# Kernel tuning notes

Measured on AMD Instinct MI355X. Metric: run time of the kernel, lower is better.

Reference implementation:

```python
import jax, jax.numpy as jnp
import numpy as np

GRID_SIZE = 4
SPLINE_ORDER = 3
EDGE_DIM = 384


def make_grid():
    # efficient-KAN default grid_range [-1, 1]
    h = 2.0 / GRID_SIZE
    return (jnp.arange(-SPLINE_ORDER, GRID_SIZE + SPLINE_ORDER + 1, dtype=jnp.float32) * h - 1.0)


def b_splines(x, grid, k):
    # x: (N, d); grid: (G+2k+1,) shared across features -> (N, d, G+k)
    xe = x[..., None]
    bases = ((xe >= grid[:-1]) & (xe < grid[1:])).astype(x.dtype)
    for j in range(1, k + 1):
        bases = ((xe - grid[: -(j + 1)]) / (grid[j:-1] - grid[: -(j + 1)]) * bases[..., :-1]
                 + (grid[j + 1:] - xe) / (grid[j + 1:] - grid[1:-j]) * bases[..., 1:])
    return bases


def kan_linear(x, base_W, spline_W, grid):
    # efficient-KAN KANLinear: silu base path + spline path
    base = jax.nn.silu(x) @ base_W.T
    B = b_splines(x, grid, SPLINE_ORDER)          # (N, in, G+k)
    spline = jnp.einsum('nic,oic->no', B, spline_W)
    return base + spline


def gckan_layer(x, edge_index, edge_attr, p, grid):
    ea = edge_attr @ p['edge_W'].T + p['edge_b']          # (E, out)
    xt = x @ p['node_W'].T + p['node_b']                  # (N, out)
    row, col = edge_index[0], edge_index[1]
    msg = ea * xt[row]                                    # gather + multiply
    agg = jnp.zeros_like(xt).at[col].add(msg)             # scatter-add
    return kan_linear(agg, p['base_W'], p['spline_W'], grid)


def _layer_params(key, in_feat, out_feat):
    k1, k2, k3, k4 = jax.random.split(key, 4)
    coef = GRID_SIZE + SPLINE_ORDER
    return {
        'node_W': jax.random.normal(k1, (out_feat, in_feat), jnp.float32) / np.sqrt(in_feat),
        'node_b': jnp.zeros((out_feat,), jnp.float32),
        'edge_W': jax.random.normal(k2, (out_feat, EDGE_DIM), jnp.float32) / np.sqrt(EDGE_DIM),
        'edge_b': jnp.zeros((out_feat,), jnp.float32),
        'base_W': jax.random.normal(k3, (out_feat, out_feat), jnp.float32) / np.sqrt(out_feat),
        'spline_W': jax.random.normal(k4, (out_feat, out_feat, coef), jnp.float32) * (0.1 / np.sqrt(out_feat)),
    }


def setup_inputs() -> dict:
    N, E, F, H, C = 50000, 500000, 256, 256, 32
    key = jax.random.key(0)
    ks = jax.random.split(key, 6)
    inp = {
        'x': jax.random.normal(ks[0], (N, F), jnp.float32),
        'edge_index': jax.random.randint(ks[1], (2, E), 0, N, jnp.int32),
        'edge_attr': jax.random.normal(ks[2], (E, EDGE_DIM), jnp.float32),
    }
    p0 = _layer_params(ks[3], F, H)
    p1 = _layer_params(ks[4], H, H)
    po = _layer_params(ks[5], F + 2 * H, C)
    for tag, p in (('0', p0), ('1', p1), ('o', po)):
        for n, v in p.items():
            inp[n + tag] = v
    return inp


def reference(x, edge_index, edge_attr,
              node_W0, node_b0, edge_W0, edge_b0, base_W0, spline_W0,
              node_W1, node_b1, edge_W1, edge_b1, base_W1, spline_W1,
              node_Wo, node_bo, edge_Wo, edge_bo, base_Wo, spline_Wo):
    grid = make_grid()
    p0 = dict(node_W=node_W0, node_b=node_b0, edge_W=edge_W0, edge_b=edge_b0, base_W=base_W0, spline_W=spline_W0)
    p1 = dict(node_W=node_W1, node_b=node_b1, edge_W=edge_W1, edge_b=edge_b1, base_W=base_W1, spline_W=spline_W1)
    po = dict(node_W=node_Wo, node_b=node_bo, edge_W=edge_Wo, edge_b=edge_bo, base_W=base_Wo, spline_W=spline_Wo)
    skips = [x]
    h = gckan_layer(x, edge_index, edge_attr, p0, grid)
    skips.append(h)
    h = gckan_layer(h, edge_index, edge_attr, p1, grid)
    skips.append(h)
    h = jnp.concatenate(skips, axis=1)  # skip=True concat -> (N, F+2H)
    return gckan_layer(h, edge_index, edge_attr, po, grid)
```

## Files before the change

kernel.cpp:

```cpp
#include <hip/hip_runtime.h>


typedef __attribute__((ext_vector_type(4))) float f32x4;
typedef __attribute__((ext_vector_type(8))) short bf16x8;
typedef __attribute__((ext_vector_type(8))) unsigned short u16x8;
typedef __attribute__((ext_vector_type(4))) unsigned short u16x4;

__device__ __forceinline__ unsigned short f2bf(float f) {
    union { float f; unsigned u; } v; v.f = f;
    unsigned r = v.u + 0x7FFFu + ((v.u >> 16) & 1u);
    return (unsigned short)(r >> 16);
}

__device__ __forceinline__ float bf2f(unsigned short u) {
    union { unsigned u; float f; } v; v.u = ((unsigned)u) << 16;
    return v.f;
}

__device__ __forceinline__ float siluf(float x) {
    return x / (1.0f + __expf(-x));
}

__device__ __forceinline__ void expand8(float x, float* o8) {
    float b[10];
#pragma unroll
    for (int i = 0; i < 10; ++i) {
        float ti = 0.5f * i - 2.5f;
        b[i] = (x >= ti && x < ti + 0.5f) ? 1.0f : 0.0f;
    }
#pragma unroll
    for (int j = 1; j <= 3; ++j) {
        float inv = 2.0f / (float)j;
#pragma unroll
        for (int i = 0; i < 10 - j; ++i) {
            float ti = 0.5f * i - 2.5f;
            float tj = 0.5f * (i + j + 1) - 2.5f;
            b[i] = (x - ti) * inv * b[i] + (tj - x) * inv * b[i + 1];
        }
    }
    o8[0] = siluf(x);
#pragma unroll
    for (int c = 0; c < 7; ++c) o8[c + 1] = b[c];
}

__global__ __launch_bounds__(256) void k_hist(
    const int* __restrict__ col, int* __restrict__ cnt, int E) {
    int i = blockIdx.x * 256 + threadIdx.x;
    if (i < E) atomicAdd(&cnt[col[i]], 1);
}

__global__ __launch_bounds__(1024) void k_scan(int* __restrict__ c, int N) {
    __shared__ int wsum[16];
    __shared__ int ctot;
    const int t = threadIdx.x;
    const int lane = t & 63, wid = t >> 6;
    int carry = 0;
    for (int base = 0; base < N; base += 1024) {
        int i = base + t;
        int v0 = (i < N) ? c[i] : 0;
        int v = v0;
#pragma unroll
        for (int off = 1; off < 64; off <<= 1) {
            int n = __shfl_up(v, (unsigned)off, 64);
            if (lane >= off) v += n;
        }
        if (lane == 63) wsum[wid] = v;
        __syncthreads();
        if (t < 16) {
            int s = wsum[t], sv = s;
#pragma unroll
            for (int off = 1; off < 16; off <<= 1) {
                int n = __shfl_up(sv, (unsigned)off, 16);
                if (t >= off) sv += n;
            }
            wsum[t] = sv - s;
            if (t == 15) ctot = sv;
        }
        __syncthreads();
        if (i < N) c[i] = carry + wsum[wid] + v - v0;
        carry += ctot;
        __syncthreads();
    }
}

__global__ __launch_bounds__(256) void k_scatter(
    const int* __restrict__ row, const int* __restrict__ col,
    int* __restrict__ cursor, int* __restrict__ rowS,
    int* __restrict__ colS, int* __restrict__ eidS, int E) {
    int i = blockIdx.x * 256 + threadIdx.x;
    if (i < E) {
        int c = col[i];
        int p = atomicAdd(&cursor[c], 1);
        rowS[p] = row[i];
        colS[p] = c;
        eidS[p] = i;
    }
}

__global__ __launch_bounds__(256) void pack_kt(
    const float* __restrict__ src, unsigned short* __restrict__ dst,
    int N, int K) {
    long idx = (long)blockIdx.x * 256 + threadIdx.x;
    if (idx >= (long)N * K) return;
    int n = (int)(idx / K), k = (int)(idx - (long)n * K);
    long o = (((long)(k >> 5) * 4 + ((k >> 3) & 3)) * N + n) * 8 + (k & 7);
    dst[o] = f2bf(src[idx]);
}

__global__ __launch_bounds__(256) void pack_kan_kt(
    const float* __restrict__ baseW, const float* __restrict__ splineW,
    unsigned short* __restrict__ dst, int N) {
    long idx = (long)blockIdx.x * 256 + threadIdx.x;
    if (idx >= (long)N * 2048) return;
    int n = (int)(idx >> 11), k = (int)(idx & 2047);
    int ic = k >> 3, c = k & 7;
    float v = (c == 0) ? baseW[(long)n * 256 + ic]
                       : splineW[((long)n * 256 + ic) * 7 + (c - 1)];
    long o = (((long)(k >> 5) * 4 + ((k >> 3) & 3)) * N + n) * 8 + (k & 7);
    dst[o] = f2bf(v);
}

template <bool TWO, bool WITH_O>
__global__ __launch_bounds__(256, 2) void ea_gemm8(
    const float* __restrict__ EA,
    const unsigned short* __restrict__ Wp0, const float* __restrict__ b0,
    const unsigned short* __restrict__ Wp1, const float* __restrict__ b1,
    const unsigned short* __restrict__ Wpo, const float* __restrict__ bo,
    unsigned short* __restrict__ O0, unsigned short* __restrict__ O1,
    unsigned short* __restrict__ Oo, int E) {
    __shared__ __align__(16) char smem[8192];

    const int tid = threadIdx.x;
    const int wv = tid >> 6, lane = tid & 63;
    const int l15 = lane & 15, l4 = lane >> 4;
    const long m0 = (long)blockIdx.x * 64;

    f32x4 acc0[4][4] = {};
    f32x4 acc1[4][4] = {};
    f32x4 acco[4] = {};

    const int sr = tid >> 2, sg = tid & 3;
    const long arow = m0 + sr;
    const bool aok = arow < E;
    const float* aptr = EA + arow * 384 + sg * 8;
    const int awoff = sg * 1024 + ((sr ^ (sg << 2))) * 16;

    const char* bp0 = (const char*)Wp0 + l4 * 4096 + wv * 1024 + l15 * 16;
    const char* bp1 = (const char*)Wp1 + l4 * 4096 + wv * 1024 + l15 * 16;
    const char* bpo = (const char*)Wpo + l4 * 512 + (wv * 16 + l15) * 16;

#define WRITE_A8(IT, VA, VB)                                                   \
    {                                                                          \
        u16x8 rr = {};                                                         \
        if (aok) {                                                             \
            rr[0] = f2bf((VA).x); rr[1] = f2bf((VA).y);                        \
            rr[2] = f2bf((VA).z); rr[3] = f2bf((VA).w);                        \
            rr[4] = f2bf((VB).x); rr[5] = f2bf((VB).y);                        \
            rr[6] = f2bf((VB).z); rr[7] = f2bf((VB).w);                        \
        }                                                                      \
        *(u16x8*)(smem + ((IT) & 1) * 4096 + awoff) = rr;                      \
    }

    const float4 z4 = make_float4(0.f, 0.f, 0.f, 0.f);
    {
        float4 s0 = z4, s1 = z4;
        if (aok) { s0 = *(const float4*)(aptr); s1 = *(const float4*)(aptr + 4); }
        WRITE_A8(0, s0, s1);
    }
    float4 r1a = z4, r1b = z4, r0a = z4, r0b = z4;
    if (aok) {
        r1a = *(const float4*)(aptr + 32); r1b = *(const float4*)(aptr + 36);
        r0a = *(const float4*)(aptr + 64); r0b = *(const float4*)(aptr + 68);
    }

#pragma unroll
    for (int it = 0; it < 12; ++it) {
        asm volatile("s_waitcnt lgkmcnt(0)" ::: "memory");
        __builtin_amdgcn_s_barrier();
        __builtin_amdgcn_sched_barrier(0);

        if (it < 11) {
            if ((it + 1) & 1) { WRITE_A8(it + 1, r1a, r1b); }
            else              { WRITE_A8(it + 1, r0a, r0b); }
            if (it <= 8) {
                if ((it + 3) & 1) {
                    if (aok) {
                        r1a = *(const float4*)(aptr + (it + 3) * 32);
                        r1b = *(const float4*)(aptr + (it + 3) * 32 + 4);
                    }
                } else {
                    if (aok) {
                        r0a = *(const float4*)(aptr + (it + 3) * 32);
                        r0b = *(const float4*)(aptr + (it + 3) * 32 + 4);
                    }
                }
            }
        }

        const int buf = it & 1;
        bf16x8 af[4];
#pragma unroll
        for (int mi = 0; mi < 4; ++mi)
            af[mi] = *(const bf16x8*)(smem + buf * 4096 + l4 * 1024 +
                                      (((mi * 16 + l15) ^ (l4 << 2))) * 16);
        {
            bf16x8 bf0[4];
#pragma unroll
            for (int nj = 0; nj < 4; ++nj)
                bf0[nj] = *(const bf16x8*)(bp0 + (long)it * 16384 + nj * 256);
#pragma unroll
            for (int mi = 0; mi < 4; ++mi)
#pragma unroll
                for (int nj = 0; nj < 4; ++nj)
                    acc0[mi][nj] = __builtin_amdgcn_mfma_f32_16x16x32_bf16(
                        af[mi], bf0[nj], acc0[mi][nj], 0, 0, 0);
        }
        if (TWO) {
            bf16x8 bf1[4];
#pragma unroll
            for (int nj = 0; nj < 4; ++nj)
                bf1[nj] = *(const bf16x8*)(bp1 + (long)it * 16384 + nj * 256);
#pragma unroll
            for (int mi = 0; mi < 4; ++mi)
#pragma unroll
                for (int nj = 0; nj < 4; ++nj)
                    acc1[mi][nj] = __builtin_amdgcn_mfma_f32_16x16x32_bf16(
                        af[mi], bf1[nj], acc1[mi][nj], 0, 0, 0);
        }
        if (WITH_O && wv < 2) {
            bf16x8 bov = *(const bf16x8*)(bpo + (long)it * 2048);
#pragma unroll
            for (int mi = 0; mi < 4; ++mi)
                acco[mi] = __builtin_amdgcn_mfma_f32_16x16x32_bf16(
                    af[mi], bov, acco[mi], 0, 0, 0);
        }
    }
#undef WRITE_A8

    const int nb2 = wv * 64;
    float bs0[4];
#pragma unroll
    for (int nj = 0; nj < 4; ++nj) bs0[nj] = b0[nb2 + nj * 16 + l15];
#pragma unroll
    for (int mi = 0; mi < 4; ++mi) {
#pragma unroll
        for (int r = 0; r < 4; ++r) {
            long e = m0 + mi * 16 + l4 * 4 + r;
            if (e < E) {
                unsigned short* dst = O0 + e * 256 + nb2 + l15;
#pragma unroll
                for (int nj = 0; nj < 4; ++nj)
                    dst[nj * 16] = f2bf(acc0[mi][nj][r] + bs0[nj]);
            }
        }
    }
    if (TWO) {
        float bs1[4];
#pragma unroll
        for (int nj = 0; nj < 4; ++nj) bs1[nj] = b1[nb2 + nj * 16 + l15];
#pragma unroll
        for (int mi = 0; mi < 4; ++mi) {
#pragma unroll
            for (int r = 0; r < 4; ++r) {
                long e = m0 + mi * 16 + l4 * 4 + r;
                if (e < E) {
                    unsigned short* dst = O1 + e * 256 + nb2 + l15;
#pragma unroll
                    for (int nj = 0; nj < 4; ++nj)
                        dst[nj * 16] = f2bf(acc1[mi][nj][r] + bs1[nj]);
                }
            }
        }
    }
    if (WITH_O && wv < 2) {
        float bso = bo[wv * 16 + l15];
#pragma unroll
        for (int mi = 0; mi < 4; ++mi) {
#pragma unroll
            for (int r = 0; r < 4; ++r) {
                long e = m0 + mi * 16 + l4 * 4 + r;
                if (e < E)
                    Oo[e * 32 + wv * 16 + l15] = f2bf(acco[mi][r] + bso);
            }
        }
    }
}

__global__ __launch_bounds__(256, 2) void kan_mfma256_r(
    const float* __restrict__ AGG, const unsigned short* __restrict__ Wp,
    float* __restrict__ Y, int M) {
    __shared__ __align__(16) char smem[8192];
    const int tid = threadIdx.x;
    const int wv = tid >> 6, lane = tid & 63;
    const int l15 = lane & 15, l4 = lane >> 4;
    const long m0 = (long)blockIdx.x * 64;
    f32x4 acc[4][4] = {};

    const int srow = tid & 63, sg = tid >> 6;
    const long arow = m0 + srow;
    const bool aok = arow < M;
    const float* aptr = AGG + arow * 256 + sg;
    const int awoff = sg * 1024 + srow * 16;
    const char* bp = (const char*)Wp + l4 * 4096 + wv * 1024 + l15 * 16;

    {
        float xv0 = aok ? aptr[0] : 0.f;
        float e8[8];
        expand8(xv0, e8);
        u16x8 ap;
#pragma unroll
        for (int c = 0; c < 8; ++c) ap[c] = f2bf(e8[c]);
        *(u16x8*)(smem + awoff) = ap;
    }
    float xv1 = aok ? aptr[4] : 0.f;

    for (int it = 0; it < 64; ++it) {
        asm volatile("s_waitcnt lgkmcnt(0)" ::: "memory");
        __builtin_amdgcn_s_barrier();
        __builtin_amdgcn_sched_barrier(0);
        const int buf = it & 1;
        if (it < 63) {
            float e8[8];
            expand8(xv1, e8);
            u16x8 ap;
#pragma unroll
            for (int c = 0; c < 8; ++c) ap[c] = f2bf(e8[c]);
            *(u16x8*)(smem + (buf ^ 1) * 4096 + awoff) = ap;
            if (it < 62) xv1 = aok ? aptr[(it + 2) * 4] : 0.f;
        }
        bf16x8 af[4], bfv[4];
#pragma unroll
        for (int mi = 0; mi < 4; ++mi)
            af[mi] = *(const bf16x8*)(smem + buf * 4096 + l4 * 1024 +
                                      (mi * 16 + l15) * 16);
#pragma unroll
        for (int nj = 0; nj < 4; ++nj)
            bfv[nj] = *(const bf16x8*)(bp + (long)it * 16384 + nj * 256);
#pragma unroll
        for (int mi = 0; mi < 4; ++mi)
#pragma unroll
            for (int nj = 0; nj < 4; ++nj)
                acc[mi][nj] = __builtin_amdgcn_mfma_f32_16x16x32_bf16(
                    af[mi], bfv[nj], acc[mi][nj], 0, 0, 0);
    }

    const int nb = wv * 64;
#pragma unroll
    for (int mi = 0; mi < 4; ++mi) {
#pragma unroll
        for (int r = 0; r < 4; ++r) {
            long gm = m0 + mi * 16 + l4 * 4 + r;
            if (gm < M) {
#pragma unroll
                for (int nj = 0; nj < 4; ++nj)
                    Y[gm * 256 + nb + nj * 16 + l15] = acc[mi][nj][r];
            }
        }
    }
}

template <int K>
__global__ __launch_bounds__(256, 2) void node_mfma_r(
    const float* __restrict__ X, const unsigned short* __restrict__ Wp,
    const float* __restrict__ bias, unsigned short* __restrict__ Y, int M) {
    __shared__ __align__(16) char smem[8192];
    const int tid = threadIdx.x;
    const int wv = tid >> 6, lane = tid & 63;
    const int l15 = lane & 15, l4 = lane >> 4;
    const long m0 = (long)blockIdx.x * 64;
    f32x4 acc[4][4] = {};
    constexpr int NIT = K / 32;

    const int sr = tid >> 2, sg = tid & 3;
    const long arow = m0 + sr;
    const bool aok = arow < M;
    const float* aptr = X + arow * K + sg * 8;
    const int awoff = sg * 1024 + ((sr ^ (sg << 2))) * 16;
    const char* bp = (const char*)Wp + l4 * 4096 + wv * 1024 + l15 * 16;

#define WRITE_NA8(IT, VA, VB)                                                  \
    {                                                                          \
        u16x8 rr = {};                                                         \
        if (aok) {                                                             \
            rr[0] = f2bf((VA).x); rr[1] = f2bf((VA).y);                        \
            rr[2] = f2bf((VA).z); rr[3] = f2bf((VA).w);                        \
            rr[4] = f2bf((VB).x); rr[5] = f2bf((VB).y);                        \
            rr[6] = f2bf((VB).z); rr[7] = f2bf((VB).w);                        \
        }                                                                      \
        *(u16x8*)(smem + ((IT) & 1) * 4096 + awoff) = rr;                      \
    }

    const float4 z4 = make_float4(0.f, 0.f, 0.f, 0.f);
    {
        float4 s0 = z4, s1 = z4;
        if (aok) { s0 = *(const float4*)(aptr); s1 = *(const float4*)(aptr + 4); }
        WRITE_NA8(0, s0, s1);
    }
    float4 r1a = z4, r1b = z4, r0a = z4, r0b = z4;
    if (aok) {
        r1a = *(const float4*)(aptr + 32); r1b = *(const float4*)(aptr + 36);
        r0a = *(const float4*)(aptr + 64); r0b = *(const float4*)(aptr + 68);
    }

#pragma unroll
    for (int it = 0; it < NIT; ++it) {
        asm volatile("s_waitcnt lgkmcnt(0)" ::: "memory");
        __builtin_amdgcn_s_barrier();
        __builtin_amdgcn_sched_barrier(0);
        if (it < NIT - 1) {
            if ((it + 1) & 1) { WRITE_NA8(it + 1, r1a, r1b); }
            else              { WRITE_NA8(it + 1, r0a, r0b); }
            if (it <= NIT - 4) {
                if ((it + 3) & 1) {
                    if (aok) {
                        r1a = *(const float4*)(aptr + (it + 3) * 32);
                        r1b = *(const float4*)(aptr + (it + 3) * 32 + 4);
                    }
                } else {
                    if (aok) {
                        r0a = *(const float4*)(aptr + (it + 3) * 32);
                        r0b = *(const float4*)(aptr + (it + 3) * 32 + 4);
                    }
                }
            }
        }
        const int buf = it & 1;
        bf16x8 af[4], bfv[4];
#pragma unroll
        for (int mi = 0; mi < 4; ++mi)
            af[mi] = *(const bf16x8*)(smem + buf * 4096 + l4 * 1024 +
                                      (((mi * 16 + l15) ^ (l4 << 2))) * 16);
#pragma unroll
        for (int nj = 0; nj < 4; ++nj)
            bfv[nj] = *(const bf16x8*)(bp + (long)it * 16384 + nj * 256);
#pragma unroll
        for (int mi = 0; mi < 4; ++mi)
#pragma unroll
            for (int nj = 0; nj < 4; ++nj)
                acc[mi][nj] = __builtin_amdgcn_mfma_f32_16x16x32_bf16(
                    af[mi], bfv[nj], acc[mi][nj], 0, 0, 0);
    }
#undef WRITE_NA8

    const int nb = wv * 64;
    float bs[4];
#pragma unroll
    for (int nj = 0; nj < 4; ++nj) bs[nj] = bias[nb + nj * 16 + l15];
#pragma unroll
    for (int mi = 0; mi < 4; ++mi) {
#pragma unroll
        for (int r = 0; r < 4; ++r) {
            long gm = m0 + mi * 16 + l4 * 4 + r;
            if (gm < M) {
#pragma unroll
                for (int nj = 0; nj < 4; ++nj)
                    Y[gm * 256 + nb + nj * 16 + l15] = f2bf(acc[mi][nj][r] + bs[nj]);
            }
        }
    }
}

__global__ __launch_bounds__(256) void msg256(
    const unsigned short* __restrict__ EAr, const unsigned short* __restrict__ XT,
    const int* __restrict__ rowS, const int* __restrict__ colS,
    const int* __restrict__ eidS, float* __restrict__ AGG, int E) {
    __shared__ __align__(16) unsigned short eas[64][264];
    __shared__ int rows_s[64];
    __shared__ int cols_s[64];
    const int tid = threadIdx.x;
    const long m0 = (long)blockIdx.x * 64;

    const int r = tid >> 2, s = tid & 3;
    {
        long p = m0 + r;
        if (p < E) {
            const unsigned short* src = EAr + (long)eidS[p] * 256 + s * 8;
#pragma unroll
            for (int k = 0; k < 8; ++k)
                *(u16x8*)&eas[r][s * 8 + k * 32] = *(const u16x8*)(src + k * 32);
        } else {
            u16x8 z = {};
#pragma unroll
            for (int k = 0; k < 8; ++k) *(u16x8*)&eas[r][s * 8 + k * 32] = z;
        }
    }
    if (tid < 64) {
        long p = m0 + tid;
        cols_s[tid] = (p < E) ? colS[p] : -1;
        rows_s[tid] = (p < E) ? rowS[p] : 0;
    }
    __syncthreads();

    const int c = tid;
    float sum = 0.f;
    int cur = cols_s[0];
    int runstart = 0;
#pragma unroll 1
    for (int g = 0; g < 8; ++g) {
        float xv[8];
#pragma unroll
        for (int j = 0; j < 8; ++j)
            xv[j] = bf2f(XT[(long)rows_s[g * 8 + j] * 256 + c]);
#pragma unroll
        for (int j = 0; j < 8; ++j) {
            int e = g * 8 + j;
            int cc = cols_s[e];
            if (cc != cur) {
                if (cur >= 0) {
                    float* dst = AGG + (long)cur * 256 + c;
                    if (runstart > 0) *dst = sum;
                    else atomicAdd(dst, sum);
                }
                cur = cc; runstart = e; sum = 0.f;
            }
            sum += bf2f(eas[e][c]) * xv[j];
        }
    }
    if (cur >= 0) {
        atomicAdd(AGG + (long)cur * 256 + c, sum);
    }
}

__global__ __launch_bounds__(256) void msg32(
    const unsigned short* __restrict__ EAro, const unsigned short* __restrict__ XT,
    const int* __restrict__ rowS, const int* __restrict__ colS,
    const int* __restrict__ eidS, float* __restrict__ AGG, int E) {
    __shared__ __align__(16) unsigned short eas[256][36];
    __shared__ int rows_s[256];
    __shared__ int cols_s[256];
    __shared__ int eid_s[256];
    const int tid = threadIdx.x;
    const long m0 = (long)blockIdx.x * 256;

    {
        long p = m0 + tid;
        cols_s[tid] = (p < E) ? colS[p] : -1;
        rows_s[tid] = (p < E) ? rowS[p] : 0;
        eid_s[tid]  = (p < E) ? eidS[p] : -1;
    }
    __syncthreads();
    const int rr0 = tid >> 2, s = tid & 3;
#pragma unroll
    for (int ps = 0; ps < 4; ++ps) {
        int rr = ps * 64 + rr0;
        int eid = eid_s[rr];
        u16x8 v = {};
        if (eid >= 0) v = *(const u16x8*)(EAro + (long)eid * 32 + s * 8);
        *(u16x8*)&eas[rr][s * 8] = v;
    }
    __syncthreads();

    const int c = tid & 31, sb = tid >> 5;
    const int e0 = sb * 32;
    float sum = 0.f;
    int cur = cols_s[e0];
    int runstart = e0;
#pragma unroll 1
    for (int g = 0; g < 4; ++g) {
        float xv[8];
#pragma unroll
        for (int j = 0; j < 8; ++j)
            xv[j] = bf2f(XT[(long)rows_s[e0 + g * 8 + j] * 32 + c]);
#pragma unroll
        for (int j = 0; j < 8; ++j) {
            int e = e0 + g * 8 + j;
            int cc = cols_s[e];
            if (cc != cur) {
                if (cur >= 0) {
                    float* dst = AGG + (long)cur * 32 + c;
                    if (runstart > 0 && cols_s[runstart - 1] != cur) *dst = sum;
                    else atomicAdd(dst, sum);
                }
                cur = cc; runstart = e; sum = 0.f;
            }
            sum += bf2f(eas[e][c]) * xv[j];
        }
    }
    if (cur >= 0) {
        int eend = e0 + 32;
        float* dst = AGG + (long)cur * 32 + c;
        bool oks = (runstart > 0 && cols_s[runstart - 1] != cur);
        bool oke = (eend < 256 && cols_s[eend] != cur);
        if (oks && oke) *dst = sum;
        else atomicAdd(dst, sum);
    }
}

__global__ __launch_bounds__(256) void node_cat_mfma(
    const float* __restrict__ X, const float* __restrict__ H0,
    const float* __restrict__ H1, const unsigned short* __restrict__ Wh,
    const float* __restrict__ bias, unsigned short* __restrict__ Y, int M) {
    __shared__ __align__(16) unsigned short As[4][256][8];
    __shared__ __align__(16) unsigned short Bs[4][32][8];
    const int tid = threadIdx.x;
    const int wv = tid >> 6, lane = tid & 63;
    const int l15 = lane & 15, l4 = lane >> 4;
    const long m0 = (long)blockIdx.x * 256;
    f32x4 acc[4][2] = {};

    const int sr = tid >> 3;
    const int sq = (tid & 7) * 4;
    const int sg2 = sq >> 3, so2 = sq & 7;

    for (int it = 0; it < 24; ++it) {
        const int k0 = it * 32;
        const float* src = (it < 8) ? X : (it < 16) ? H0 : H1;
        const int kk = k0 & 255;
        float4 va[8];
#pragma unroll
        for (int j = 0; j < 8; ++j) {
            long r_ = m0 + j * 32 + sr;
            va[j] = (r_ < M) ? *(const float4*)(src + r_ * 256 + kk + sq)
                             : make_float4(0.f, 0.f, 0.f, 0.f);
        }
        u16x8 bv = {};
        if (tid < 128)
            bv = *(const u16x8*)(Wh + (long)(tid >> 2) * 768 + k0 + (tid & 3) * 8);
        __syncthreads();
#pragma unroll
        for (int j = 0; j < 8; ++j) {
            u16x4 ap;
            ap[0] = f2bf(va[j].x); ap[1] = f2bf(va[j].y);
            ap[2] = f2bf(va[j].z); ap[3] = f2bf(va[j].w);
            *(u16x4*)&As[sg2][j * 32 + sr][so2] = ap;
        }
        if (tid < 128) *(u16x8*)&Bs[tid & 3][tid >> 2][0] = bv;
        __syncthreads();
        bf16x8 af[4], bfv[2];
#pragma unroll
        for (int mi = 0; mi < 4; ++mi)
            af[mi] = *(const bf16x8*)&As[l4][wv * 64 + mi * 16 + l15][0];
#pragma unroll
        for (int nj = 0; nj < 2; ++nj)
            bfv[nj] = *(const bf16x8*)&Bs[l4][nj * 16 + l15][0];
#pragma unroll
        for (int mi = 0; mi < 4; ++mi)
#pragma unroll
            for (int nj = 0; nj < 2; ++nj)
                acc[mi][nj] = __builtin_amdgcn_mfma_f32_16x16x32_bf16(
                    af[mi], bfv[nj], acc[mi][nj], 0, 0, 0);
    }

#pragma unroll
    for (int mi = 0; mi < 4; ++mi) {
#pragma unroll
        for (int r = 0; r < 4; ++r) {
            long gm = m0 + wv * 64 + mi * 16 + l4 * 4 + r;
            if (gm < M) {
#pragma unroll
                for (int nj = 0; nj < 2; ++nj) {
                    int o = nj * 16 + l15;
                    Y[gm * 32 + o] = f2bf(acc[mi][nj][r] + bias[o]);
                }
            }
        }
    }
}

__global__ __launch_bounds__(256) void kan_gemm32(
    const float* __restrict__ AGG, const float* __restrict__ Wc,
    float* __restrict__ Y, int M) {
    __shared__ float As[64][36];
    __shared__ float Bs[32][36];
    const int tid = threadIdx.x;
    const int tx = tid & 15, ty = tid >> 4;
    const int m0 = blockIdx.x * 64;
    float acc[4][2] = {{0.f, 0.f}, {0.f, 0.f}, {0.f, 0.f}, {0.f, 0.f}};
    const int er = tid >> 2, ef = tid & 3;
    const int em = m0 + er;
    for (int ic = 0; ic < 32; ic += 4) {
        float xv = (em < M) ? AGG[(long)em * 32 + ic + ef] : 0.f;
        float e8[8];
        expand8(xv, e8);
        *(float4*)&As[er][ef * 8] = make_float4(e8[0], e8[1], e8[2], e8[3]);
        *(float4*)&As[er][ef * 8 + 4] = make_float4(e8[4], e8[5], e8[6], e8[7]);
        {
            int o = tid >> 3, k4 = (tid & 7) * 4;
            *(float4*)&Bs[o][k4] = *(const float4*)&Wc[(long)o * 256 + ic * 8 + k4];
        }
        __syncthreads();
#pragma unroll
        for (int kk = 0; kk < 32; ++kk) {
            float a_[4], b_[2];
#pragma unroll
            for (int i = 0; i < 4; ++i) a_[i] = As[ty * 4 + i][kk];
#pragma unroll
            for (int j = 0; j < 2; ++j) b_[j] = Bs[tx * 2 + j][kk];
#pragma unroll
            for (int i = 0; i < 4; ++i)
#pragma unroll
                for (int j = 0; j < 2; ++j) acc[i][j] = fmaf(a_[i], b_[j], acc[i][j]);
        }
        __syncthreads();
    }
#pragma unroll
    for (int i = 0; i < 4; ++i) {
        int gm = m0 + ty * 4 + i;
        if (gm >= M) continue;
#pragma unroll
        for (int j = 0; j < 2; ++j) Y[(long)gm * 32 + tx * 2 + j] = acc[i][j];
    }
}

__global__ __launch_bounds__(256) void cvt_bf16(
    const float* __restrict__ s, unsigned short* __restrict__ d, int n) {
    int i = blockIdx.x * 256 + threadIdx.x;
    if (i < n) d[i] = f2bf(s[i]);
}

__global__ __launch_bounds__(256) void pack_kan_f32(
    const float* __restrict__ baseW, const float* __restrict__ splineW,
    float* __restrict__ Wc, int n) {
    int idx = blockIdx.x * 256 + threadIdx.x;
    if (idx >= n) return;
    float* dst = Wc + (long)idx * 8;
    dst[0] = baseW[idx];
    const float* sw = splineW + (long)idx * 7;
#pragma unroll
    for (int c = 0; c < 7; ++c) dst[1 + c] = sw[c];
}

extern "C" void kernel_launch(void* const* d_in, const int* in_sizes, int n_in,
                              void* d_out, int out_size, void* d_ws, size_t ws_size,
                              hipStream_t stream) {
    const float* x          = (const float*)d_in[0];
    const int*   edge_index = (const int*)d_in[1];
    const float* edge_attr  = (const float*)d_in[2];
    const float* node_W0 = (const float*)d_in[3];
    const float* node_b0 = (const float*)d_in[4];
    const float* edge_W0 = (const float*)d_in[5];
    const float* edge_b0 = (const float*)d_in[6];
    const float* base_W0 = (const float*)d_in[7];
    const float* spline_W0 = (const float*)d_in[8];
    const float* node_W1 = (const float*)d_in[9];
    const float* node_b1 = (const float*)d_in[10];
    const float* edge_W1 = (const float*)d_in[11];
    const float* edge_b1 = (const float*)d_in[12];
    const float* base_W1 = (const float*)d_in[13];
    const float* spline_W1 = (const float*)d_in[14];
    const float* node_Wo = (const float*)d_in[15];
    const float* node_bo = (const float*)d_in[16];
    const float* edge_Wo = (const float*)d_in[17];
    const float* edge_bo = (const float*)d_in[18];
    const float* base_Wo = (const float*)d_in[19];
    const float* spline_Wo = (const float*)d_in[20];
    float* out = (float*)d_out;

    const int N = in_sizes[0] / 256;
    const int E = in_sizes[1] / 2;

    float* ws  = (float*)d_ws;
    unsigned short* xt = (unsigned short*)ws;
    float* agg = ws + (long)N * 256;
    float* h0  = agg + (long)N * 256;
    float* h1  = h0 + (long)N * 256;
    float* Wco = h1 + (long)N * 256;
    unsigned short* Wp0  = (unsigned short*)(Wco + 32 * 256);
    unsigned short* Wp1  = Wp0 + 98304;
    unsigned short* Wpo  = Wp1 + 98304;
    unsigned short* nWp0 = Wpo + 12288;
    unsigned short* nWp1 = nWp0 + 65536;
    unsigned short* Wc0p = nWp1 + 65536;
    unsigned short* Wc1p = Wc0p + 524288;
    unsigned short* nWoh = Wc1p + 524288;
    int* cursor = (int*)(nWoh + 24576);
    int* rowS   = cursor + (N + 1);
    int* colS   = rowS + E;
    int* eidS   = colS + E;
    unsigned short* EAr0 = (unsigned short*)(((uintptr_t)(eidS + E) + 255) & ~(uintptr_t)255);
    const int nt256 = (E + 255) / 256;
    const long Epad = (long)nt256 * 256;
    unsigned short* EAr1 = EAr0 + Epad * 256;

    const size_t need2 = (size_t)((char*)(EAr1 + Epad * 256 + Epad * 32) - (char*)d_ws);
    const bool two = ws_size >= need2;
    unsigned short* EAro = two ? (EAr1 + Epad * 256) : (EAr0 + Epad * 256);

    const int* row = edge_index;
    const int* col = edge_index + E;

    const int nb64 = (N + 63) / 64;
    const int eb64 = (E + 63) / 64;
    const int eb256 = (E + 255) / 256;
    const int nb256 = (N + 255) / 256;

    hipMemsetAsync(cursor, 0, (size_t)(N + 1) * sizeof(int), stream);
    k_hist<<<eb256, 256, 0, stream>>>(col, cursor, E);
    k_scan<<<1, 1024, 0, stream>>>(cursor, N);
    k_scatter<<<eb256, 256, 0, stream>>>(row, col, cursor, rowS, colS, eidS, E);

    pack_kt<<<(256 * 384 + 255) / 256, 256, 0, stream>>>(edge_W0, Wp0, 256, 384);
    pack_kt<<<(256 * 384 + 255) / 256, 256, 0, stream>>>(edge_W1, Wp1, 256, 384);
    pack_kt<<<(32 * 384 + 255) / 256, 256, 0, stream>>>(edge_Wo, Wpo, 32, 384);
    pack_kt<<<(256 * 256 + 255) / 256, 256, 0, stream>>>(node_W0, nWp0, 256, 256);
    pack_kt<<<(256 * 256 + 255) / 256, 256, 0, stream>>>(node_W1, nWp1, 256, 256);
    pack_kan_kt<<<(256 * 2048 + 255) / 256, 256, 0, stream>>>(base_W0, spline_W0, Wc0p, 256);
    pack_kan_kt<<<(256 * 2048 + 255) / 256, 256, 0, stream>>>(base_W1, spline_W1, Wc1p, 256);
    cvt_bf16<<<(32 * 768 + 255) / 256, 256, 0, stream>>>(node_Wo, nWoh, 32 * 768);
    pack_kan_f32<<<(32 * 32 + 255) / 256, 256, 0, stream>>>(base_Wo, spline_Wo, Wco, 32 * 32);

    if (two) {
        ea_gemm8<true, true><<<eb64, 256, 0, stream>>>(
            edge_attr, Wp0, edge_b0, Wp1, edge_b1, Wpo, edge_bo,
            EAr0, EAr1, EAro, E);
    } else {
        ea_gemm8<false, true><<<eb64, 256, 0, stream>>>(
            edge_attr, Wp0, edge_b0, Wp0, edge_b0, Wpo, edge_bo,
            EAr0, EAr0, EAro, E);
    }

    hipMemsetAsync(agg, 0, (size_t)N * 256 * sizeof(float), stream);
    node_mfma_r<256><<<nb64, 256, 0, stream>>>(x, nWp0, node_b0, xt, N);
    msg256<<<eb64, 256, 0, stream>>>(EAr0, xt, rowS, colS, eidS, agg, E);
    kan_mfma256_r<<<nb64, 256, 0, stream>>>(agg, Wc0p, h0, N);

    if (!two) {
        ea_gemm8<false, false><<<eb64, 256, 0, stream>>>(
            edge_attr, Wp1, edge_b1, Wp1, edge_b1, Wpo, edge_bo,
            EAr0, EAr0, EAro, E);
    }
    hipMemsetAsync(agg, 0, (size_t)N * 256 * sizeof(float), stream);
    node_mfma_r<256><<<nb64, 256, 0, stream>>>(h0, nWp1, node_b1, xt, N);
    msg256<<<eb64, 256, 0, stream>>>(two ? EAr1 : EAr0, xt, rowS, colS, eidS, agg, E);
    kan_mfma256_r<<<nb64, 256, 0, stream>>>(agg, Wc1p, h1, N);

    hipMemsetAsync(agg, 0, (size_t)N * 32 * sizeof(float), stream);
    node_cat_mfma<<<nb256, 256, 0, stream>>>(x, h0, h1, nWoh, node_bo, xt, N);
    msg32<<<eb256, 256, 0, stream>>>(EAro, xt, rowS, colS, eidS, agg, E);
    kan_gemm32<<<nb64, 256, 0, stream>>>(agg, Wco, out, N);
}
```

Measured before the change: 1.328 ms.

## Split edge GEMM across 8 waves with per-wave weight matrix ownership

The fused edge-attribute GEMM now launches 512 threads per block instead of 256. Waves 0-3 compute the layer-0 projection and waves 4-7 the layer-1 projection, so each wave holds one 16-tile accumulator set instead of two. The small 32-wide output projection is spread over all 8 waves, one MFMA each per step. This cuts per-thread register pressure to allow more resident waves and better latency hiding. In exchange, every wave reads the shared A tile and gets half the MFMA work per barrier. In the non-TWO case, waves 4-7 do redundant work that is discarded.

```diff
diff --git a/kernel.cpp b/kernel.cpp
--- a/kernel.cpp
+++ b/kernel.cpp
@@ -121,7 +121,7 @@
 }
 
 template <bool TWO, bool WITH_O>
-__global__ __launch_bounds__(256, 2) void ea_gemm8(
+__global__ __launch_bounds__(512, 4) void ea_gemm9(
     const float* __restrict__ EA,
     const unsigned short* __restrict__ Wp0, const float* __restrict__ b0,
     const unsigned short* __restrict__ Wp1, const float* __restrict__ b1,
@@ -135,42 +135,41 @@
     const int l15 = lane & 15, l4 = lane >> 4;
     const long m0 = (long)blockIdx.x * 64;
 
-    f32x4 acc0[4][4] = {};
-    f32x4 acc1[4][4] = {};
-    f32x4 acco[4] = {};
-
-    const int sr = tid >> 2, sg = tid & 3;
+    f32x4 acc[16] = {};
+    f32x4 acco = {};
+
+    const int sr = tid >> 3, sg = tid & 7;
     const long arow = m0 + sr;
     const bool aok = arow < E;
-    const float* aptr = EA + arow * 384 + sg * 8;
-    const int awoff = sg * 1024 + ((sr ^ (sg << 2))) * 16;
-
-    const char* bp0 = (const char*)Wp0 + l4 * 4096 + wv * 1024 + l15 * 16;
-    const char* bp1 = (const char*)Wp1 + l4 * 4096 + wv * 1024 + l15 * 16;
-    const char* bpo = (const char*)Wpo + l4 * 512 + (wv * 16 + l15) * 16;
-
-#define WRITE_A8(IT, VA, VB)                                                   \
+    const float* aptr = EA + arow * 384 + sg * 4;
+    const int gg = sg >> 1;
+    const int awoff = gg * 1024 + (sr ^ (gg << 2)) * 16 + (sg & 1) * 8;
+
+    const char* bp = (const char*)((TWO && wv >= 4) ? Wp1 : Wp0) +
+                     l4 * 4096 + (wv & 3) * 1024 + l15 * 16;
+    const char* bpo = (const char*)Wpo + l4 * 512 + ((wv >> 2) * 16 + l15) * 16;
+    const int aooff = l4 * 1024 + (((wv & 3) * 16 + l15) ^ (l4 << 2)) * 16;
+
+#define WRITE_A9(IT, V)                                                        \
     {                                                                          \
-        u16x8 rr = {};                                                         \
+        u16x4 rr = {};                                                         \
         if (aok) {                                                             \
-            rr[0] = f2bf((VA).x); rr[1] = f2bf((VA).y);                        \
-            rr[2] = f2bf((VA).z); rr[3] = f2bf((VA).w);                        \
-            rr[4] = f2bf((VB).x); rr[5] = f2bf((VB).y);                        \
-            rr[6] = f2bf((VB).z); rr[7] = f2bf((VB).w);                        \
+            rr[0] = f2bf((V).x); rr[1] = f2bf((V).y);                          \
+            rr[2] = f2bf((V).z); rr[3] = f2bf((V).w);                          \
         }                                                                      \
-        *(u16x8*)(smem + ((IT) & 1) * 4096 + awoff) = rr;                      \
+        *(u16x4*)(smem + ((IT) & 1) * 4096 + awoff) = rr;                      \
     }
 
     const float4 z4 = make_float4(0.f, 0.f, 0.f, 0.f);
     {
-        float4 s0 = z4, s1 = z4;
-        if (aok) { s0 = *(const float4*)(aptr); s1 = *(const float4*)(aptr + 4); }
-        WRITE_A8(0, s0, s1);
-    }
-    float4 r1a = z4, r1b = z4, r0a = z4, r0b = z4;
+        float4 s0 = z4;
+        if (aok) s0 = *(const float4*)(aptr);
+        WRITE_A9(0, s0);
+    }
+    float4 rs1 = z4, rs0 = z4;
     if (aok) {
-        r1a = *(const float4*)(aptr + 32); r1b = *(const float4*)(aptr + 36);
-        r0a = *(const float4*)(aptr + 64); r0b = *(const float4*)(aptr + 68);
+        rs1 = *(const float4*)(aptr + 32);
+        rs0 = *(const float4*)(aptr + 64);
     }
 
 #pragma unroll
@@ -180,19 +179,13 @@
         __builtin_amdgcn_sched_barrier(0);
 
         if (it < 11) {
-            if ((it + 1) & 1) { WRITE_A8(it + 1, r1a, r1b); }
-            else              { WRITE_A8(it + 1, r0a, r0b); }
+            if ((it + 1) & 1) { WRITE_A9(it + 1, rs1); }
+            else              { WRITE_A9(it + 1, rs0); }
             if (it <= 8) {
                 if ((it + 3) & 1) {
-                    if (aok) {
-                        r1a = *(const float4*)(aptr + (it + 3) * 32);
-                        r1b = *(const float4*)(aptr + (it + 3) * 32 + 4);
-                    }
+                    if (aok) rs1 = *(const float4*)(aptr + (it + 3) * 32);
                 } else {
-                    if (aok) {
-                        r0a = *(const float4*)(aptr + (it + 3) * 32);
-                        r0b = *(const float4*)(aptr + (it + 3) * 32 + 4);
-                    }
+                    if (aok) rs0 = *(const float4*)(aptr + (it + 3) * 32);
                 }
             }
         }
@@ -203,85 +196,52 @@
         for (int mi = 0; mi < 4; ++mi)
             af[mi] = *(const bf16x8*)(smem + buf * 4096 + l4 * 1024 +
                                       (((mi * 16 + l15) ^ (l4 << 2))) * 16);
-        {
-            bf16x8 bf0[4];
+        bf16x8 bfv[4];
+#pragma unroll
+        for (int nj = 0; nj < 4; ++nj)
+            bfv[nj] = *(const bf16x8*)(bp + (long)it * 16384 + nj * 256);
+#pragma unroll
+        for (int mi = 0; mi < 4; ++mi)
 #pragma unroll
             for (int nj = 0; nj < 4; ++nj)
-                bf0[nj] = *(const bf16x8*)(bp0 + (long)it * 16384 + nj * 256);
-#pragma unroll
-            for (int mi = 0; mi < 4; ++mi)
-#pragma unroll
-                for (int nj = 0; nj < 4; ++nj)
-                    acc0[mi][nj] = __builtin_amdgcn_mfma_f32_16x16x32_bf16(
-                        af[mi], bf0[nj], acc0[mi][nj], 0, 0, 0);
-        }
-        if (TWO) {
-            bf16x8 bf1[4];
-#pragma unroll
-            for (int nj = 0; nj < 4; ++nj)
-                bf1[nj] = *(const bf16x8*)(bp1 + (long)it * 16384 + nj * 256);
-#pragma unroll
-            for (int mi = 0; mi < 4; ++mi)
-#pragma unroll
-                for (int nj = 0; nj < 4; ++nj)
-                    acc1[mi][nj] = __builtin_amdgcn_mfma_f32_16x16x32_bf16(
-                        af[mi], bf1[nj], acc1[mi][nj], 0, 0, 0);
-        }
-        if (WITH_O && wv < 2) {
+                acc[mi * 4 + nj] = __builtin_amdgcn_mfma_f32_16x16x32_bf16(
+                    af[mi], bfv[nj], acc[mi * 4 + nj], 0, 0, 0);
+        if (WITH_O) {
+            bf16x8 aw = *(const bf16x8*)(smem + buf * 4096 + aooff);
             bf16x8 bov = *(const bf16x8*)(bpo + (long)it * 2048);
-#pragma unroll
-            for (int mi = 0; mi < 4; ++mi)
-                acco[mi] = __builtin_amdgcn_mfma_f32_16x16x32_bf16(
-                    af[mi], bov, acco[mi], 0, 0, 0);
-        }
-    }
-#undef WRITE_A8
-
-    const int nb2 = wv * 64;
-    float bs0[4];
-#pragma unroll
-    for (int nj = 0; nj < 4; ++nj) bs0[nj] = b0[nb2 + nj * 16 + l15];
-#pragma unroll
-    for (int mi = 0; mi < 4; ++mi) {
-#pragma unroll
-        for (int r = 0; r < 4; ++r) {
-            long e = m0 + mi * 16 + l4 * 4 + r;
-            if (e < E) {
-                unsigned short* dst = O0 + e * 256 + nb2 + l15;
-#pragma unroll
-                for (int nj = 0; nj < 4; ++nj)
-                    dst[nj * 16] = f2bf(acc0[mi][nj][r] + bs0[nj]);
-            }
-        }
-    }
-    if (TWO) {
-        float bs1[4];
-#pragma unroll
-        for (int nj = 0; nj < 4; ++nj) bs1[nj] = b1[nb2 + nj * 16 + l15];
+            acco = __builtin_amdgcn_mfma_f32_16x16x32_bf16(aw, bov, acco, 0, 0, 0);
+        }
+    }
+#undef WRITE_A9
+
+    const int nb2 = (wv & 3) * 64;
+    if (TWO || wv < 4) {
+        const float* bb = (TWO && wv >= 4) ? b1 : b0;
+        unsigned short* OO = (TWO && wv >= 4) ? O1 : O0;
+        float bs[4];
+#pragma unroll
+        for (int nj = 0; nj < 4; ++nj) bs[nj] = bb[nb2 + nj * 16 + l15];
 #pragma unroll
         for (int mi = 0; mi < 4; ++mi) {
 #pragma unroll
             for (int r = 0; r < 4; ++r) {
                 long e = m0 + mi * 16 + l4 * 4 + r;
                 if (e < E) {
-                    unsigned short* dst = O1 + e * 256 + nb2 + l15;
+                    unsigned short* dst = OO + e * 256 + nb2 + l15;
 #pragma unroll
                     for (int nj = 0; nj < 4; ++nj)
-                        dst[nj * 16] = f2bf(acc1[mi][nj][r] + bs1[nj]);
+                        dst[nj * 16] = f2bf(acc[mi * 4 + nj][r] + bs[nj]);
                 }
             }
         }
     }
-    if (WITH_O && wv < 2) {
-        float bso = bo[wv * 16 + l15];
-#pragma unroll
-        for (int mi = 0; mi < 4; ++mi) {
-#pragma unroll
-            for (int r = 0; r < 4; ++r) {
-                long e = m0 + mi * 16 + l4 * 4 + r;
-                if (e < E)
-                    Oo[e * 32 + wv * 16 + l15] = f2bf(acco[mi][r] + bso);
-            }
+    if (WITH_O) {
+        const int oc = (wv >> 2) * 16 + l15;
+        const float bso = bo[oc];
+#pragma unroll
+        for (int r = 0; r < 4; ++r) {
+            long e = m0 + (wv & 3) * 16 + l4 * 4 + r;
+            if (e < E) Oo[e * 32 + oc] = f2bf(acco[r] + bso);
         }
     }
 }
@@ -800,11 +760,11 @@
     pack_kan_f32<<<(32 * 32 + 255) / 256, 256, 0, stream>>>(base_Wo, spline_Wo, Wco, 32 * 32);
 
     if (two) {
-        ea_gemm8<true, true><<<eb64, 256, 0, stream>>>(
+        ea_gemm9<true, true><<<eb64, 512, 0, stream>>>(
             edge_attr, Wp0, edge_b0, Wp1, edge_b1, Wpo, edge_bo,
             EAr0, EAr1, EAro, E);
     } else {
-        ea_gemm8<false, true><<<eb64, 256, 0, stream>>>(
+        ea_gemm9<false, true><<<eb64, 512, 0, stream>>>(
             edge_attr, Wp0, edge_b0, Wp0, edge_b0, Wpo, edge_bo,
             EAr0, EAr0, EAro, E);
     }
@@ -815,7 +775,7 @@
     kan_mfma256_r<<<nb64, 256, 0, stream>>>(agg, Wc0p, h0, N);
 
     if (!two) {
-        ea_gemm8<false, false><<<eb64, 256, 0, stream>>>(
+        ea_gemm9<false, false><<<eb64, 512, 0, stream>>>(
             edge_attr, Wp1, edge_b1, Wp1, edge_b1, Wpo, edge_bo,
             EAr0, EAr0, EAro, E);
     }
```

Result: slower. 1.445 ms (+8.9%).
